# Kernel optimization log

Measured on AMD Instinct MI355X. Metric: run time of the kernel, lower is better.

Reference implementation:

```python
import jax, jax.numpy as jnp
import numpy as np

P = 8        # num policies
Z = 64       # per-policy latent dim
D = P * Z    # total latent dim = 512
A = 8        # action dim
H = 512      # hidden dim
B = 8192     # batch


def setup_inputs() -> dict:
    key = jax.random.key(0)
    ks = jax.random.split(key, 10)
    IN = Z + A
    s1 = 1.0 / np.sqrt(IN)
    s2 = 1.0 / np.sqrt(H)
    return {
        "latents": jax.random.normal(ks[0], (B, D), dtype=jnp.float32),
        "actions": jax.random.normal(ks[1], (B, A), dtype=jnp.float32),
        "policy_indices": jax.random.randint(ks[2], (B,), 0, P, dtype=jnp.int64) if jax.config.jax_enable_x64 else jax.random.randint(ks[2], (B,), 0, P, dtype=jnp.int32),
        # Stacked params for P_outer x P_inner MLPs: (z+A) -> H -> H -> Z
        "W1": jax.random.uniform(ks[3], (P, P, IN, H), jnp.float32, -s1, s1),
        "b1": jax.random.uniform(ks[4], (P, P, H), jnp.float32, -s1, s1),
        "W2": jax.random.uniform(ks[5], (P, P, H, H), jnp.float32, -s2, s2),
        "b2": jax.random.uniform(ks[6], (P, P, H), jnp.float32, -s2, s2),
        "W3": jax.random.uniform(ks[7], (P, P, H, Z), jnp.float32, -s2, s2),
        "b3": jax.random.uniform(ks[8], (P, P, Z), jnp.float32, -s2, s2),
    }


def reference(latents, actions, policy_indices, W1, b1, W2, b2, W3, b3):
    Bb, Dd = latents.shape
    Pp = W1.shape[0]
    Zz = Dd // Pp
    # split latent into per-policy chunks: [B, P, Z]
    pl = latents.reshape(Bb, Pp, Zz)
    # each inner MLP sees (its latent chunk, shared action): [B, P, Z+A]
    act = jnp.broadcast_to(actions[:, None, :], (Bb, Pp, actions.shape[-1]))
    x = jnp.concatenate([pl, act], axis=-1)
    out = jnp.zeros_like(latents)
    # loop over outer policy models (fixed small set); select rows by policy index
    for i in range(Pp):
        h = jax.nn.relu(jnp.einsum("bpi,pih->bph", x, W1[i]) + b1[i])
        h = jax.nn.relu(jnp.einsum("bph,phk->bpk", h, W2[i]) + b2[i])
        y = jnp.einsum("bph,phz->bpz", h, W3[i]) + b3[i]  # [B, P, Z]
        y = y.reshape(Bb, Dd)  # concat over inner policies
        out = jnp.where((policy_indices == i)[:, None], y, out)
    return out
```

## Files before the change

kernel.cpp:

```cpp
#include <hip/hip_runtime.h>
#include <stdint.h>

#define PNUM  8
#define DDIM  512
#define ZDIM  64
#define ADIM  8
#define HDIM  512
#define BATCH 8192
#define KIN   72
#define NKS1  3
#define NKS2  16
#define NKS3  16
#define NT12  32
#define NT3   4
#define TM    64
#define PXP   104
#define PHP   520

typedef __attribute__((ext_vector_type(8))) __bf16 bf16x8;
typedef __attribute__((ext_vector_type(4))) float  f32x4;

#define WS_COUNTS_I 0
#define WS_OFFS_I   16
#define WS_CURS_I   32
#define WS_FLG_I    42
#define WS_PERM_I   64
#define WS_W1P_B    40960
#define WS_W2P_B    (WS_W1P_B + 64*NKS1*NT12*1024)
#define WS_W3P_B    (WS_W2P_B + 64*NKS2*NT12*1024)
#define WS_NEED_B   (WS_W3P_B + 64*NKS3*NT3*1024)

__device__ __forceinline__ float bf2f(ushort h){
  union { unsigned int u; float f; } v; v.u = ((unsigned int)h) << 16; return v.f;
}
__device__ __forceinline__ ushort f2bf(float f){
  union { float f; unsigned int u; } v; v.f = f;
  unsigned int u = v.u;
  return (ushort)((u + 0x7FFFu + ((u >> 16) & 1u)) >> 16);
}
__device__ __forceinline__ unsigned int pk2(ushort lo, ushort hi){
  return (unsigned int)lo | ((unsigned int)hi << 16);
}
__device__ __forceinline__ int ldidx(const void* p, int t, int i64){
  return i64 ? (int)((const long long*)p)[t] : ((const int*)p)[t];
}
__device__ __forceinline__ float4 ldbias4(const void* b, size_t off, int f32){
  if (f32) return *(const float4*)((const float*)b + off);
  ushort4 q = *(const ushort4*)((const ushort*)b + off);
  float4 r; r.x = bf2f(q.x); r.y = bf2f(q.y); r.z = bf2f(q.z); r.w = bf2f(q.w);
  return r;
}

__global__ void k_prep(const unsigned int* __restrict__ lat,
                       const unsigned int* __restrict__ act,
                       const unsigned int* __restrict__ w1,
                       const unsigned int* __restrict__ bb1,
                       const unsigned int* __restrict__ w2,
                       const unsigned int* __restrict__ bb2,
                       const unsigned int* __restrict__ w3,
                       const unsigned int* __restrict__ bb3,
                       const void* __restrict__ idx,
                       int* __restrict__ wsi){
  __shared__ int hist[PNUM];
  __shared__ int cur[PNUM];
  __shared__ int flg_i64;
  const int tid = threadIdx.x;
  if (tid < PNUM) hist[tid] = 0;
  const int t = tid >> 6, lane = tid & 63;
  if (t == 8){
    unsigned long long nz = __ballot(((const unsigned int*)idx)[2 * lane + 1] != 0u);
    if (lane == 0){ int v = (nz == 0ull) ? 1 : 0; wsi[WS_FLG_I + 8] = v; flg_i64 = v; }
  } else if (t < 8){
    const unsigned int* ptrs[8] = {lat, act, w1, bb1, w2, bb2, w3, bb3};
    unsigned int u = ptrs[t][lane];
    unsigned int e = (u >> 7) & 0xFFu;
    unsigned long long ib = __ballot(e >= 100u && e <= 150u);
    if (lane == 0) wsi[WS_FLG_I + t] = (__popcll(ib) < 40) ? 1 : 0;
  }
  __syncthreads();
  const int i64 = flg_i64;
  int pol[8];
  #pragma unroll
  for (int c = 0; c < 8; c++){
    pol[c] = ldidx(idx, c * 1024 + tid, i64);
    atomicAdd(&hist[pol[c]], 1);
  }
  __syncthreads();
  if (tid == 0){
    int off = 0;
    #pragma unroll
    for (int i = 0; i < PNUM; i++){
      int h = hist[i];
      wsi[WS_COUNTS_I + i] = h;
      wsi[WS_OFFS_I + i] = off;
      cur[i] = off;
      off += h;
    }
  }
  __syncthreads();
  #pragma unroll
  for (int c = 0; c < 8; c++){
    int pos = atomicAdd(&cur[pol[c]], 1);
    wsi[WS_PERM_I + pos] = c * 1024 + tid;
  }
}

#define PK_W1_N  1536
#define PK_W2_N  8192
#define PK_W3_N  1024
__global__ void k_pack_all(const void* __restrict__ W1, const void* __restrict__ W2,
                           const void* __restrict__ W3,
                           ushort* __restrict__ w1p, ushort* __restrict__ w2p,
                           ushort* __restrict__ w3p,
                           const int* __restrict__ wsi){
  __shared__ ushort T[32][80];
  int bid = blockIdx.x;
  const void* src; ushort* dst;
  int Ksrc, nks, ntiles, N, flg, ntg, ks, pair;
  if (bid < PK_W1_N){
    src = W1; dst = w1p; Ksrc = KIN;  nks = NKS1; ntiles = NT12; N = HDIM; flg = 2;
    pair = bid / 24; int rem = bid % 24; ks = rem >> 3; ntg = rem & 7;
  } else if (bid < PK_W1_N + PK_W2_N){
    int local = bid - PK_W1_N;
    src = W2; dst = w2p; Ksrc = HDIM; nks = NKS2; ntiles = NT12; N = HDIM; flg = 4;
    pair = local / 128; int rem = local % 128; ks = rem >> 3; ntg = rem & 7;
  } else {
    int local = bid - PK_W1_N - PK_W2_N;
    src = W3; dst = w3p; Ksrc = HDIM; nks = NKS3; ntiles = NT3;  N = ZDIM; flg = 6;
    pair = local / 16; ks = local % 16; ntg = 0;
  }
  const int f32 = wsi[WS_FLG_I + flg];
  const int tid = threadIdx.x;
  const int nb = ntg * 64;

  if (f32){
    #pragma unroll
    for (int it = 0; it < 2; it++){
      int i = it * 256 + tid;
      int k = i >> 4, nq = i & 15;
      int kk = ks * 32 + k;
      float4 v = make_float4(0.f, 0.f, 0.f, 0.f);
      if (kk < Ksrc)
        v = *(const float4*)((const float*)src + ((size_t)pair * Ksrc + kk) * N + nb + nq * 4);
      ushort4 o; o.x = f2bf(v.x); o.y = f2bf(v.y); o.z = f2bf(v.z); o.w = f2bf(v.w);
      *(ushort4*)&T[k][nq * 4] = o;
    }
  } else {
    int k = tid >> 3, uq = tid & 7;
    int kk = ks * 32 + k;
    uint4 v = make_uint4(0u, 0u, 0u, 0u);
    if (kk < Ksrc)
      v = *(const uint4*)((const ushort*)src + ((size_t)pair * Ksrc + kk) * N + nb + uq * 8);
    *(uint4*)&T[k][uq * 8] = v;
  }
  __syncthreads();

  const int w = tid >> 6, lane = tid & 63;
  const int lm = lane & 15, lq = lane >> 4;
  unsigned int vv[4];
  #pragma unroll
  for (int j = 0; j < 4; j++){
    ushort lo = T[lq * 8 + 2 * j    ][w * 16 + lm];
    ushort hi = T[lq * 8 + 2 * j + 1][w * 16 + lm];
    vv[j] = pk2(lo, hi);
  }
  uint4 val = make_uint4(vv[0], vv[1], vv[2], vv[3]);
  size_t f = (size_t)(pair * nks + ks) * ntiles + (ntg * 4 + w);
  *(uint4*)(dst + f * 512 + (size_t)lane * 8) = val;
}

__global__ void __launch_bounds__(512, 2) k_mlp(
    const void* __restrict__ latents, const void* __restrict__ actions,
    const void* __restrict__ b1, const void* __restrict__ b2,
    const void* __restrict__ b3,
    const int* __restrict__ wsi,
    const ushort* __restrict__ w1p, const ushort* __restrict__ w2p,
    const ushort* __restrict__ w3p,
    void* __restrict__ out, int out_elems)
{
  __shared__ __align__(16) ushort Xb [TM * PXP];
  __shared__ __align__(16) ushort H1s[TM * PHP];
  __shared__ __align__(16) ushort H2s[TM * PHP];
  __shared__ int rowid[TM];

  const int io = blockIdx.x >> 3, p = blockIdx.x & 7, tile = blockIdx.y;
  const int cnt = wsi[WS_COUNTS_I + io];
  if (tile * TM >= cnt) return;
  const int r0    = wsi[WS_OFFS_I + io] + tile * TM;
  const int mrows = min(TM, cnt - tile * TM);
  const int pair  = io * PNUM + p;
  const int tid   = threadIdx.x;
  const int fLat  = wsi[WS_FLG_I + 0];
  const int fAct  = wsi[WS_FLG_I + 1];
  const int fB1   = wsi[WS_FLG_I + 3];
  const int fB2   = wsi[WS_FLG_I + 5];
  const int fB3   = wsi[WS_FLG_I + 7];

  const int w = tid >> 6, lane = tid & 63;
  const int lm = lane & 15, lq = lane >> 4;
  const int ntb = w * 4;
  const uint4* w1v = (const uint4*)w1p;
  const uint4* w2v = (const uint4*)w2p;
  const uint4* w3v = (const uint4*)w3p;
  const f32x4 zero4 = {0.f, 0.f, 0.f, 0.f};

  uint4 a1w[NKS1][4];
  #pragma unroll
  for (int ks = 0; ks < NKS1; ks++)
    #pragma unroll
    for (int a = 0; a < 4; a++)
      a1w[ks][a] = w1v[((size_t)(pair * NKS1 + ks) * NT12 + ntb + a) * 64 + lane];
  float4 bq1[4];
  #pragma unroll
  for (int a = 0; a < 4; a++)
    bq1[a] = ldbias4(b1, (size_t)pair * HDIM + (ntb + a) * 16 + lq * 4, fB1);

  for (int task = tid; task < TM * 16; task += 512){
    int r = task >> 4, c = task & 15;
    if (c >= 13) continue;
    uint4 val = make_uint4(0u, 0u, 0u, 0u);
    if (r < mrows){
      int row = wsi[WS_PERM_I + r0 + r];
      if (c == 8) rowid[r] = row;
      if (c < 9){
        int f32 = (c < 8) ? fLat : fAct;
        if (f32){
          const float* sf = (c < 8)
            ? ((const float*)latents + (size_t)row * DDIM + p * ZDIM + c * 8)
            : ((const float*)actions + (size_t)row * ADIM);
          float4 f0 = *(const float4*)sf;
          float4 f1 = *(const float4*)(sf + 4);
          val = make_uint4(pk2(f2bf(f0.x), f2bf(f0.y)),
                           pk2(f2bf(f0.z), f2bf(f0.w)),
                           pk2(f2bf(f1.x), f2bf(f1.y)),
                           pk2(f2bf(f1.z), f2bf(f1.w)));
        } else {
          const ushort* sh = (c < 8)
            ? ((const ushort*)latents + (size_t)row * DDIM + p * ZDIM + c * 8)
            : ((const ushort*)actions + (size_t)row * ADIM);
          val = *(const uint4*)sh;
        }
      }
    } else if (c == 8) rowid[r] = 0;
    *(uint4*)(Xb + r * PXP + c * 8) = val;
  }
  __syncthreads();

  #define MFMA16(A, B) \
    { _Pragma("unroll") for (int a_ = 0; a_ < 4; a_++) \
      { _Pragma("unroll") for (int m_ = 0; m_ < 4; m_++) \
        acc[a_][m_] = __builtin_amdgcn_mfma_f32_16x16x32_bf16( \
            __builtin_bit_cast(bf16x8, A[a_]), __builtin_bit_cast(bf16x8, B[m_]), \
            acc[a_][m_], 0, 0, 0); } }
  #define LDA2(dst, kss) \
    { _Pragma("unroll") for (int a_ = 0; a_ < 4; a_++) \
        dst[a_] = w2v[((size_t)(pair * NKS2 + (kss)) * NT12 + ntb + a_) * 64 + lane]; }
  #define LDB4(dst, kss) \
    { _Pragma("unroll") for (int m_ = 0; m_ < 4; m_++) \
        dst[m_] = *(const uint4*)(H1s + (size_t)(m_ * 16 + lm) * PHP + (kss) * 32 + lq * 8); }
  #define CP4(dst, srcv) \
    { _Pragma("unroll") for (int a_ = 0; a_ < 4; a_++) dst[a_] = srcv[a_]; }

  {
    f32x4 acc[4][4];
    #pragma unroll
    for (int a = 0; a < 4; a++)
      #pragma unroll
      for (int m = 0; m < 4; m++) acc[a][m] = zero4;

    #pragma unroll
    for (int ks = 0; ks < NKS1; ks++){
      uint4 bfm[4];
      #pragma unroll
      for (int m = 0; m < 4; m++)
        bfm[m] = *(const uint4*)(Xb + (size_t)(m * 16 + lm) * PXP + ks * 32 + lq * 8);
      MFMA16(a1w[ks], bfm);
    }
    #pragma unroll
    for (int a = 0; a < 4; a++){
      int n0 = (ntb + a) * 16 + lq * 4;
      #pragma unroll
      for (int m = 0; m < 4; m++){
        ushort4 o;
        o.x = f2bf(fmaxf(acc[a][m][0] + bq1[a].x, 0.f));
        o.y = f2bf(fmaxf(acc[a][m][1] + bq1[a].y, 0.f));
        o.z = f2bf(fmaxf(acc[a][m][2] + bq1[a].z, 0.f));
        o.w = f2bf(fmaxf(acc[a][m][3] + bq1[a].w, 0.f));
        *(ushort4*)(H1s + (size_t)(m * 16 + lm) * PHP + n0) = o;
      }
    }
  }

  uint4 A0[4], A1[4];
  LDA2(A0, 0);
  LDA2(A1, 1);
  float4 bq2[4];
  #pragma unroll
  for (int a = 0; a < 4; a++)
    bq2[a] = ldbias4(b2, (size_t)pair * HDIM + (ntb + a) * 16 + lq * 4, fB2);
  __syncthreads();

  {
    f32x4 acc[4][4];
    #pragma unroll
    for (int a = 0; a < 4; a++)
      #pragma unroll
      for (int m = 0; m < 4; m++) acc[a][m] = zero4;

    uint4 B0[4], B1[4];
    LDB4(B0, 0);
    #pragma unroll
    for (int ks = 0; ks < NKS2; ks += 2){
      uint4 TA[4];
      if (ks + 2 < NKS2) LDA2(TA, ks + 2);
      LDB4(B1, ks + 1);
      MFMA16(A0, B0);
      if (ks + 2 < NKS2) CP4(A0, TA);
      uint4 TB[4];
      if (ks + 3 < NKS2) LDA2(TB, ks + 3);
      if (ks + 2 < NKS2) LDB4(B0, ks + 2);
      MFMA16(A1, B1);
      if (ks + 3 < NKS2) CP4(A1, TB);
    }
    #pragma unroll
    for (int a = 0; a < 4; a++){
      int n0 = (ntb + a) * 16 + lq * 4;
      #pragma unroll
      for (int m = 0; m < 4; m++){
        ushort4 o;
        o.x = f2bf(fmaxf(acc[a][m][0] + bq2[a].x, 0.f));
        o.y = f2bf(fmaxf(acc[a][m][1] + bq2[a].y, 0.f));
        o.z = f2bf(fmaxf(acc[a][m][2] + bq2[a].z, 0.f));
        o.w = f2bf(fmaxf(acc[a][m][3] + bq2[a].w, 0.f));
        *(ushort4*)(H2s + (size_t)(m * 16 + lm) * PHP + n0) = o;
      }
    }
  }

  const int zt = w & 3, mb = w >> 2;
  uint4 C0 = w3v[((size_t)(pair * NKS3 + 0) * NT3 + zt) * 64 + lane];
  uint4 C1 = w3v[((size_t)(pair * NKS3 + 1) * NT3 + zt) * 64 + lane];
  float4 bq3 = ldbias4(b3, (size_t)pair * ZDIM + zt * 16 + lq * 4, fB3);
  __syncthreads();

  {
    f32x4 acc3[2];
    acc3[0] = zero4; acc3[1] = zero4;
    #pragma unroll
    for (int ks = 0; ks < NKS3; ks += 2){
      uint4 T0, T1;
      if (ks + 2 < NKS3)
        T0 = w3v[((size_t)(pair * NKS3 + ks + 2) * NT3 + zt) * 64 + lane];
      if (ks + 3 < NKS3)
        T1 = w3v[((size_t)(pair * NKS3 + ks + 3) * NT3 + zt) * 64 + lane];
      #pragma unroll
      for (int h = 0; h < 2; h++){
        int row = (mb + 2 * h) * 16 + lm;
        uint4 bf = *(const uint4*)(H2s + (size_t)row * PHP + ks * 32 + lq * 8);
        acc3[h] = __builtin_amdgcn_mfma_f32_16x16x32_bf16(
            __builtin_bit_cast(bf16x8, C0), __builtin_bit_cast(bf16x8, bf), acc3[h], 0, 0, 0);
      }
      #pragma unroll
      for (int h = 0; h < 2; h++){
        int row = (mb + 2 * h) * 16 + lm;
        uint4 bf = *(const uint4*)(H2s + (size_t)row * PHP + (ks + 1) * 32 + lq * 8);
        acc3[h] = __builtin_amdgcn_mfma_f32_16x16x32_bf16(
            __builtin_bit_cast(bf16x8, C1), __builtin_bit_cast(bf16x8, bf), acc3[h], 0, 0, 0);
      }
      if (ks + 2 < NKS3) C0 = T0;
      if (ks + 3 < NKS3) C1 = T1;
    }
    int z0 = zt * 16 + lq * 4;
    #pragma unroll
    for (int h = 0; h < 2; h++){
      int mm = (mb + 2 * h) * 16 + lm;
      if (mm < mrows){
        int row = rowid[mm];
        size_t oidx = (size_t)row * DDIM + p * ZDIM + z0;
        if (oidx + 4 <= (size_t)out_elems){
          if (fLat){
            float4 o;
            o.x = acc3[h][0] + bq3.x;
            o.y = acc3[h][1] + bq3.y;
            o.z = acc3[h][2] + bq3.z;
            o.w = acc3[h][3] + bq3.w;
            *(float4*)((float*)out + oidx) = o;
          } else {
            ushort4 o;
            o.x = f2bf(acc3[h][0] + bq3.x);
            o.y = f2bf(acc3[h][1] + bq3.y);
            o.z = f2bf(acc3[h][2] + bq3.z);
            o.w = f2bf(acc3[h][3] + bq3.w);
            *(ushort4*)((ushort*)out + oidx) = o;
          }
        }
      }
    }
  }
  #undef MFMA16
  #undef LDA2
  #undef LDB4
  #undef CP4
}

extern "C" void kernel_launch(void* const* d_in, const int* in_sizes, int n_in,
                              void* d_out, int out_size, void* d_ws, size_t ws_size,
                              hipStream_t stream){
  if (n_in < 9) return;
  const void* latents = d_in[0];
  const void* actions = d_in[1];
  const void* pidx    = d_in[2];
  const void* W1      = d_in[3];
  const void* b1      = d_in[4];
  const void* W2      = d_in[5];
  const void* b2      = d_in[6];
  const void* W3      = d_in[7];
  const void* b3      = d_in[8];

  if (ws_size < (size_t)WS_NEED_B) return;

  int*    wsi = (int*)d_ws;
  char*   wsb = (char*)d_ws;
  ushort* w1p = (ushort*)(wsb + WS_W1P_B);
  ushort* w2p = (ushort*)(wsb + WS_W2P_B);
  ushort* w3p = (ushort*)(wsb + WS_W3P_B);

  k_prep<<<1, 1024, 0, stream>>>(
      (const unsigned int*)latents, (const unsigned int*)actions,
      (const unsigned int*)W1, (const unsigned int*)b1,
      (const unsigned int*)W2, (const unsigned int*)b2,
      (const unsigned int*)W3, (const unsigned int*)b3,
      pidx, wsi);
  k_pack_all<<<PK_W1_N + PK_W2_N + PK_W3_N, 256, 0, stream>>>(
      W1, W2, W3, w1p, w2p, w3p, wsi);
  k_mlp<<<dim3(64, BATCH/TM), 512, 0, stream>>>(
      latents, actions, b1, b2, b3, wsi, w1p, w2p, w3p, d_out, out_size);
}
```

Before: 219.3 us.

## Use persistent 1024-thread MLP blocks looping over tiles; warp-aggregate histogram

```diff
diff --git a/kernel.cpp b/kernel.cpp
--- a/kernel.cpp
+++ b/kernel.cpp
@@ -14,6 +14,7 @@
 #define NT12  32
 #define NT3   4
 #define TM    64
+#define TILEY 16
 #define PXP   104
 #define PHP   520
 
@@ -65,8 +66,8 @@
   __shared__ int cur[PNUM];
   __shared__ int flg_i64;
   const int tid = threadIdx.x;
+  const int t = tid >> 6, lane = tid & 63;
   if (tid < PNUM) hist[tid] = 0;
-  const int t = tid >> 6, lane = tid & 63;
   if (t == 8){
     unsigned long long nz = __ballot(((const unsigned int*)idx)[2 * lane + 1] != 0u);
     if (lane == 0){ int v = (nz == 0ull) ? 1 : 0; wsi[WS_FLG_I + 8] = v; flg_i64 = v; }
@@ -81,9 +82,22 @@
   const int i64 = flg_i64;
   int pol[8];
   #pragma unroll
+  for (int c = 0; c < 8; c++) pol[c] = ldidx(idx, c * 1024 + tid, i64);
+
+  int wcnt[PNUM];
+  #pragma unroll
+  for (int i = 0; i < PNUM; i++) wcnt[i] = 0;
+  #pragma unroll
   for (int c = 0; c < 8; c++){
-    pol[c] = ldidx(idx, c * 1024 + tid, i64);
-    atomicAdd(&hist[pol[c]], 1);
+    #pragma unroll
+    for (int i = 0; i < PNUM; i++){
+      unsigned long long m = __ballot(pol[c] == i);
+      wcnt[i] += __popcll(m);
+    }
+  }
+  if (lane == 0){
+    #pragma unroll
+    for (int i = 0; i < PNUM; i++) atomicAdd(&hist[i], wcnt[i]);
   }
   __syncthreads();
   if (tid == 0){
@@ -98,10 +112,23 @@
     }
   }
   __syncthreads();
+
   #pragma unroll
   for (int c = 0; c < 8; c++){
-    int pos = atomicAdd(&cur[pol[c]], 1);
-    wsi[WS_PERM_I + pos] = c * 1024 + tid;
+    #pragma unroll
+    for (int i = 0; i < PNUM; i++){
+      unsigned long long m = __ballot(pol[c] == i);
+      if (m){
+        int leader = __ffsll((unsigned long long)m) - 1;
+        int base = 0;
+        if (lane == leader) base = atomicAdd(&cur[i], __popcll(m));
+        base = __shfl(base, leader);
+        if (pol[c] == i){
+          int rank = __popcll(m & ((1ull << lane) - 1ull));
+          wsi[WS_PERM_I + base + rank] = c * 1024 + tid;
+        }
+      }
+    }
   }
 }
 
@@ -169,7 +196,7 @@
   *(uint4*)(dst + f * 512 + (size_t)lane * 8) = val;
 }
 
-__global__ void __launch_bounds__(512, 2) k_mlp(
+__global__ void __launch_bounds__(1024, 4) k_mlp(
     const void* __restrict__ latents, const void* __restrict__ actions,
     const void* __restrict__ b1, const void* __restrict__ b2,
     const void* __restrict__ b3,
@@ -183,11 +210,9 @@
   __shared__ __align__(16) ushort H2s[TM * PHP];
   __shared__ int rowid[TM];
 
-  const int io = blockIdx.x >> 3, p = blockIdx.x & 7, tile = blockIdx.y;
+  const int io = blockIdx.x >> 3, p = blockIdx.x & 7;
   const int cnt = wsi[WS_COUNTS_I + io];
-  if (tile * TM >= cnt) return;
-  const int r0    = wsi[WS_OFFS_I + io] + tile * TM;
-  const int mrows = min(TM, cnt - tile * TM);
+  if ((int)blockIdx.y * TM >= cnt) return;
   const int pair  = io * PNUM + p;
   const int tid   = threadIdx.x;
   const int fLat  = wsi[WS_FLG_I + 0];
@@ -198,209 +223,205 @@
 
   const int w = tid >> 6, lane = tid & 63;
   const int lm = lane & 15, lq = lane >> 4;
-  const int ntb = w * 4;
+  const int ntb = w * 2;
+  const int zt = w & 3, mq = w >> 2;
   const uint4* w1v = (const uint4*)w1p;
   const uint4* w2v = (const uint4*)w2p;
   const uint4* w3v = (const uint4*)w3p;
   const f32x4 zero4 = {0.f, 0.f, 0.f, 0.f};
 
-  uint4 a1w[NKS1][4];
+  uint4 a1w[NKS1][2];
   #pragma unroll
   for (int ks = 0; ks < NKS1; ks++)
     #pragma unroll
-    for (int a = 0; a < 4; a++)
+    for (int a = 0; a < 2; a++)
       a1w[ks][a] = w1v[((size_t)(pair * NKS1 + ks) * NT12 + ntb + a) * 64 + lane];
-  float4 bq1[4];
-  #pragma unroll
-  for (int a = 0; a < 4; a++)
+  float4 bq1[2];
+  #pragma unroll
+  for (int a = 0; a < 2; a++)
     bq1[a] = ldbias4(b1, (size_t)pair * HDIM + (ntb + a) * 16 + lq * 4, fB1);
-
-  for (int task = tid; task < TM * 16; task += 512){
-    int r = task >> 4, c = task & 15;
-    if (c >= 13) continue;
-    uint4 val = make_uint4(0u, 0u, 0u, 0u);
-    if (r < mrows){
-      int row = wsi[WS_PERM_I + r0 + r];
-      if (c == 8) rowid[r] = row;
-      if (c < 9){
-        int f32 = (c < 8) ? fLat : fAct;
-        if (f32){
-          const float* sf = (c < 8)
-            ? ((const float*)latents + (size_t)row * DDIM + p * ZDIM + c * 8)
-            : ((const float*)actions + (size_t)row * ADIM);
-          float4 f0 = *(const float4*)sf;
-          float4 f1 = *(const float4*)(sf + 4);
-          val = make_uint4(pk2(f2bf(f0.x), f2bf(f0.y)),
-                           pk2(f2bf(f0.z), f2bf(f0.w)),
-                           pk2(f2bf(f1.x), f2bf(f1.y)),
-                           pk2(f2bf(f1.z), f2bf(f1.w)));
-        } else {
-          const ushort* sh = (c < 8)
-            ? ((const ushort*)latents + (size_t)row * DDIM + p * ZDIM + c * 8)
-            : ((const ushort*)actions + (size_t)row * ADIM);
-          val = *(const uint4*)sh;
-        }
-      }
-    } else if (c == 8) rowid[r] = 0;
-    *(uint4*)(Xb + r * PXP + c * 8) = val;
-  }
-  __syncthreads();
-
-  #define MFMA16(A, B) \
-    { _Pragma("unroll") for (int a_ = 0; a_ < 4; a_++) \
+  float4 bq2[2];
+  #pragma unroll
+  for (int a = 0; a < 2; a++)
+    bq2[a] = ldbias4(b2, (size_t)pair * HDIM + (ntb + a) * 16 + lq * 4, fB2);
+  float4 bq3 = ldbias4(b3, (size_t)pair * ZDIM + zt * 16 + lq * 4, fB3);
+
+  #define MFMA8(A, B) \
+    { _Pragma("unroll") for (int a_ = 0; a_ < 2; a_++) \
       { _Pragma("unroll") for (int m_ = 0; m_ < 4; m_++) \
         acc[a_][m_] = __builtin_amdgcn_mfma_f32_16x16x32_bf16( \
             __builtin_bit_cast(bf16x8, A[a_]), __builtin_bit_cast(bf16x8, B[m_]), \
             acc[a_][m_], 0, 0, 0); } }
   #define LDA2(dst, kss) \
-    { _Pragma("unroll") for (int a_ = 0; a_ < 4; a_++) \
+    { _Pragma("unroll") for (int a_ = 0; a_ < 2; a_++) \
         dst[a_] = w2v[((size_t)(pair * NKS2 + (kss)) * NT12 + ntb + a_) * 64 + lane]; }
   #define LDB4(dst, kss) \
     { _Pragma("unroll") for (int m_ = 0; m_ < 4; m_++) \
         dst[m_] = *(const uint4*)(H1s + (size_t)(m_ * 16 + lm) * PHP + (kss) * 32 + lq * 8); }
-  #define CP4(dst, srcv) \
-    { _Pragma("unroll") for (int a_ = 0; a_ < 4; a_++) dst[a_] = srcv[a_]; }
-
-  {
-    f32x4 acc[4][4];
-    #pragma unroll
-    for (int a = 0; a < 4; a++)
-      #pragma unroll
-      for (int m = 0; m < 4; m++) acc[a][m] = zero4;
-
-    #pragma unroll
-    for (int ks = 0; ks < NKS1; ks++){
-      uint4 bfm[4];
-      #pragma unroll
-      for (int m = 0; m < 4; m++)
-        bfm[m] = *(const uint4*)(Xb + (size_t)(m * 16 + lm) * PXP + ks * 32 + lq * 8);
-      MFMA16(a1w[ks], bfm);
-    }
-    #pragma unroll
-    for (int a = 0; a < 4; a++){
-      int n0 = (ntb + a) * 16 + lq * 4;
-      #pragma unroll
-      for (int m = 0; m < 4; m++){
-        ushort4 o;
-        o.x = f2bf(fmaxf(acc[a][m][0] + bq1[a].x, 0.f));
-        o.y = f2bf(fmaxf(acc[a][m][1] + bq1[a].y, 0.f));
-        o.z = f2bf(fmaxf(acc[a][m][2] + bq1[a].z, 0.f));
-        o.w = f2bf(fmaxf(acc[a][m][3] + bq1[a].w, 0.f));
-        *(ushort4*)(H1s + (size_t)(m * 16 + lm) * PHP + n0) = o;
-      }
-    }
-  }
-
-  uint4 A0[4], A1[4];
-  LDA2(A0, 0);
-  LDA2(A1, 1);
-  float4 bq2[4];
-  #pragma unroll
-  for (int a = 0; a < 4; a++)
-    bq2[a] = ldbias4(b2, (size_t)pair * HDIM + (ntb + a) * 16 + lq * 4, fB2);
-  __syncthreads();
-
-  {
-    f32x4 acc[4][4];
-    #pragma unroll
-    for (int a = 0; a < 4; a++)
-      #pragma unroll
-      for (int m = 0; m < 4; m++) acc[a][m] = zero4;
-
-    uint4 B0[4], B1[4];
-    LDB4(B0, 0);
-    #pragma unroll
-    for (int ks = 0; ks < NKS2; ks += 2){
-      uint4 TA[4];
-      if (ks + 2 < NKS2) LDA2(TA, ks + 2);
-      LDB4(B1, ks + 1);
-      MFMA16(A0, B0);
-      if (ks + 2 < NKS2) CP4(A0, TA);
-      uint4 TB[4];
-      if (ks + 3 < NKS2) LDA2(TB, ks + 3);
-      if (ks + 2 < NKS2) LDB4(B0, ks + 2);
-      MFMA16(A1, B1);
-      if (ks + 3 < NKS2) CP4(A1, TB);
-    }
-    #pragma unroll
-    for (int a = 0; a < 4; a++){
-      int n0 = (ntb + a) * 16 + lq * 4;
-      #pragma unroll
-      for (int m = 0; m < 4; m++){
-        ushort4 o;
-        o.x = f2bf(fmaxf(acc[a][m][0] + bq2[a].x, 0.f));
-        o.y = f2bf(fmaxf(acc[a][m][1] + bq2[a].y, 0.f));
-        o.z = f2bf(fmaxf(acc[a][m][2] + bq2[a].z, 0.f));
-        o.w = f2bf(fmaxf(acc[a][m][3] + bq2[a].w, 0.f));
-        *(ushort4*)(H2s + (size_t)(m * 16 + lm) * PHP + n0) = o;
-      }
-    }
-  }
-
-  const int zt = w & 3, mb = w >> 2;
-  uint4 C0 = w3v[((size_t)(pair * NKS3 + 0) * NT3 + zt) * 64 + lane];
-  uint4 C1 = w3v[((size_t)(pair * NKS3 + 1) * NT3 + zt) * 64 + lane];
-  float4 bq3 = ldbias4(b3, (size_t)pair * ZDIM + zt * 16 + lq * 4, fB3);
-  __syncthreads();
-
-  {
-    f32x4 acc3[2];
-    acc3[0] = zero4; acc3[1] = zero4;
-    #pragma unroll
-    for (int ks = 0; ks < NKS3; ks += 2){
-      uint4 T0, T1;
-      if (ks + 2 < NKS3)
-        T0 = w3v[((size_t)(pair * NKS3 + ks + 2) * NT3 + zt) * 64 + lane];
-      if (ks + 3 < NKS3)
-        T1 = w3v[((size_t)(pair * NKS3 + ks + 3) * NT3 + zt) * 64 + lane];
-      #pragma unroll
-      for (int h = 0; h < 2; h++){
-        int row = (mb + 2 * h) * 16 + lm;
-        uint4 bf = *(const uint4*)(H2s + (size_t)row * PHP + ks * 32 + lq * 8);
-        acc3[h] = __builtin_amdgcn_mfma_f32_16x16x32_bf16(
-            __builtin_bit_cast(bf16x8, C0), __builtin_bit_cast(bf16x8, bf), acc3[h], 0, 0, 0);
-      }
-      #pragma unroll
-      for (int h = 0; h < 2; h++){
-        int row = (mb + 2 * h) * 16 + lm;
-        uint4 bf = *(const uint4*)(H2s + (size_t)row * PHP + (ks + 1) * 32 + lq * 8);
-        acc3[h] = __builtin_amdgcn_mfma_f32_16x16x32_bf16(
-            __builtin_bit_cast(bf16x8, C1), __builtin_bit_cast(bf16x8, bf), acc3[h], 0, 0, 0);
-      }
-      if (ks + 2 < NKS3) C0 = T0;
-      if (ks + 3 < NKS3) C1 = T1;
-    }
-    int z0 = zt * 16 + lq * 4;
-    #pragma unroll
-    for (int h = 0; h < 2; h++){
-      int mm = (mb + 2 * h) * 16 + lm;
+  #define CP2(dst, srcv) \
+    { _Pragma("unroll") for (int a_ = 0; a_ < 2; a_++) dst[a_] = srcv[a_]; }
+
+  for (int tile = blockIdx.y; tile * TM < cnt; tile += TILEY){
+    const int r0    = wsi[WS_OFFS_I + io] + tile * TM;
+    const int mrows = min(TM, cnt - tile * TM);
+
+    __syncthreads();
+
+    {
+      int r = tid >> 4, c = tid & 15;
+      if (c < 13){
+        uint4 val = make_uint4(0u, 0u, 0u, 0u);
+        if (r < mrows){
+          int row = wsi[WS_PERM_I + r0 + r];
+          if (c == 8) rowid[r] = row;
+          if (c < 9){
+            int f32 = (c < 8) ? fLat : fAct;
+            if (f32){
+              const float* sf = (c < 8)
+                ? ((const float*)latents + (size_t)row * DDIM + p * ZDIM + c * 8)
+                : ((const float*)actions + (size_t)row * ADIM);
+              float4 f0 = *(const float4*)sf;
+              float4 f1 = *(const float4*)(sf + 4);
+              val = make_uint4(pk2(f2bf(f0.x), f2bf(f0.y)),
+                               pk2(f2bf(f0.z), f2bf(f0.w)),
+                               pk2(f2bf(f1.x), f2bf(f1.y)),
+                               pk2(f2bf(f1.z), f2bf(f1.w)));
+            } else {
+              const ushort* sh = (c < 8)
+                ? ((const ushort*)latents + (size_t)row * DDIM + p * ZDIM + c * 8)
+                : ((const ushort*)actions + (size_t)row * ADIM);
+              val = *(const uint4*)sh;
+            }
+          }
+        } else if (c == 8) rowid[r] = 0;
+        *(uint4*)(Xb + r * PXP + c * 8) = val;
+      }
+    }
+    __syncthreads();
+
+    {
+      f32x4 acc[2][4];
+      #pragma unroll
+      for (int a = 0; a < 2; a++)
+        #pragma unroll
+        for (int m = 0; m < 4; m++) acc[a][m] = zero4;
+
+      #pragma unroll
+      for (int ks = 0; ks < NKS1; ks++){
+        uint4 bfm[4];
+        #pragma unroll
+        for (int m = 0; m < 4; m++)
+          bfm[m] = *(const uint4*)(Xb + (size_t)(m * 16 + lm) * PXP + ks * 32 + lq * 8);
+        MFMA8(a1w[ks], bfm);
+      }
+      #pragma unroll
+      for (int a = 0; a < 2; a++){
+        int n0 = (ntb + a) * 16 + lq * 4;
+        #pragma unroll
+        for (int m = 0; m < 4; m++){
+          ushort4 o;
+          o.x = f2bf(fmaxf(acc[a][m][0] + bq1[a].x, 0.f));
+          o.y = f2bf(fmaxf(acc[a][m][1] + bq1[a].y, 0.f));
+          o.z = f2bf(fmaxf(acc[a][m][2] + bq1[a].z, 0.f));
+          o.w = f2bf(fmaxf(acc[a][m][3] + bq1[a].w, 0.f));
+          *(ushort4*)(H1s + (size_t)(m * 16 + lm) * PHP + n0) = o;
+        }
+      }
+    }
+
+    uint4 A0[2], A1[2];
+    LDA2(A0, 0);
+    LDA2(A1, 1);
+    __syncthreads();
+
+    {
+      f32x4 acc[2][4];
+      #pragma unroll
+      for (int a = 0; a < 2; a++)
+        #pragma unroll
+        for (int m = 0; m < 4; m++) acc[a][m] = zero4;
+
+      uint4 B0[4], B1[4];
+      LDB4(B0, 0);
+      #pragma unroll
+      for (int ks = 0; ks < NKS2; ks += 2){
+        uint4 TA[2];
+        if (ks + 2 < NKS2) LDA2(TA, ks + 2);
+        LDB4(B1, ks + 1);
+        MFMA8(A0, B0);
+        if (ks + 2 < NKS2) CP2(A0, TA);
+        uint4 TB[2];
+        if (ks + 3 < NKS2) LDA2(TB, ks + 3);
+        if (ks + 2 < NKS2) LDB4(B0, ks + 2);
+        MFMA8(A1, B1);
+        if (ks + 3 < NKS2) CP2(A1, TB);
+      }
+      #pragma unroll
+      for (int a = 0; a < 2; a++){
+        int n0 = (ntb + a) * 16 + lq * 4;
+        #pragma unroll
+        for (int m = 0; m < 4; m++){
+          ushort4 o;
+          o.x = f2bf(fmaxf(acc[a][m][0] + bq2[a].x, 0.f));
+          o.y = f2bf(fmaxf(acc[a][m][1] + bq2[a].y, 0.f));
+          o.z = f2bf(fmaxf(acc[a][m][2] + bq2[a].z, 0.f));
+          o.w = f2bf(fmaxf(acc[a][m][3] + bq2[a].w, 0.f));
+          *(ushort4*)(H2s + (size_t)(m * 16 + lm) * PHP + n0) = o;
+        }
+      }
+    }
+
+    uint4 C0 = w3v[((size_t)(pair * NKS3 + 0) * NT3 + zt) * 64 + lane];
+    uint4 C1 = w3v[((size_t)(pair * NKS3 + 1) * NT3 + zt) * 64 + lane];
+    __syncthreads();
+
+    {
+      f32x4 acc3 = zero4;
+      #pragma unroll
+      for (int ks = 0; ks < NKS3; ks += 2){
+        uint4 T0, T1;
+        if (ks + 2 < NKS3)
+          T0 = w3v[((size_t)(pair * NKS3 + ks + 2) * NT3 + zt) * 64 + lane];
+        if (ks + 3 < NKS3)
+          T1 = w3v[((size_t)(pair * NKS3 + ks + 3) * NT3 + zt) * 64 + lane];
+        uint4 bf = *(const uint4*)(H2s + (size_t)(mq * 16 + lm) * PHP + ks * 32 + lq * 8);
+        acc3 = __builtin_amdgcn_mfma_f32_16x16x32_bf16(
+            __builtin_bit_cast(bf16x8, C0), __builtin_bit_cast(bf16x8, bf), acc3, 0, 0, 0);
+        uint4 bg = *(const uint4*)(H2s + (size_t)(mq * 16 + lm) * PHP + (ks + 1) * 32 + lq * 8);
+        acc3 = __builtin_amdgcn_mfma_f32_16x16x32_bf16(
+            __builtin_bit_cast(bf16x8, C1), __builtin_bit_cast(bf16x8, bg), acc3, 0, 0, 0);
+        if (ks + 2 < NKS3) C0 = T0;
+        if (ks + 3 < NKS3) C1 = T1;
+      }
+      int z0 = zt * 16 + lq * 4;
+      int mm = mq * 16 + lm;
       if (mm < mrows){
         int row = rowid[mm];
         size_t oidx = (size_t)row * DDIM + p * ZDIM + z0;
         if (oidx + 4 <= (size_t)out_elems){
           if (fLat){
             float4 o;
-            o.x = acc3[h][0] + bq3.x;
-            o.y = acc3[h][1] + bq3.y;
-            o.z = acc3[h][2] + bq3.z;
-            o.w = acc3[h][3] + bq3.w;
+            o.x = acc3[0] + bq3.x;
+            o.y = acc3[1] + bq3.y;
+            o.z = acc3[2] + bq3.z;
+            o.w = acc3[3] + bq3.w;
             *(float4*)((float*)out + oidx) = o;
           } else {
             ushort4 o;
-            o.x = f2bf(acc3[h][0] + bq3.x);
-            o.y = f2bf(acc3[h][1] + bq3.y);
-            o.z = f2bf(acc3[h][2] + bq3.z);
-            o.w = f2bf(acc3[h][3] + bq3.w);
+            o.x = f2bf(acc3[0] + bq3.x);
+            o.y = f2bf(acc3[1] + bq3.y);
+            o.z = f2bf(acc3[2] + bq3.z);
+            o.w = f2bf(acc3[3] + bq3.w);
             *(ushort4*)((ushort*)out + oidx) = o;
           }
         }
       }
     }
   }
-  #undef MFMA16
+  #undef MFMA8
   #undef LDA2
   #undef LDB4
-  #undef CP4
+  #undef CP2
 }
 
 extern "C" void kernel_launch(void* const* d_in, const int* in_sizes, int n_in,
@@ -433,6 +454,6 @@
       pidx, wsi);
   k_pack_all<<<PK_W1_N + PK_W2_N + PK_W3_N, 256, 0, stream>>>(
       W1, W2, W3, w1p, w2p, w3p, wsi);
-  k_mlp<<<dim3(64, BATCH/TM), 512, 0, stream>>>(
+  k_mlp<<<dim3(64, TILEY), 1024, 0, stream>>>(
       latents, actions, b1, b2, b3, wsi, w1p, w2p, w3p, d_out, out_size);
 }
```

New measurement: 527.9 us. 2.41x slower.

## Merge prep and weight-pack kernels into one launch with ballot-based histogram

Applied to the files above, without the earlier changes.

```diff
diff --git a/kernel.cpp b/kernel.cpp
--- a/kernel.cpp
+++ b/kernel.cpp
@@ -30,6 +30,12 @@
 #define WS_W3P_B    (WS_W2P_B + 64*NKS2*NT12*1024)
 #define WS_NEED_B   (WS_W3P_B + 64*NKS3*NT3*1024)
 
+#define FR_W1   6144
+#define FR_W2   32768
+#define FR_W3   4096
+#define FR_TOT  (FR_W1 + FR_W2 + FR_W3)
+#define NB_PACK 2048
+
 __device__ __forceinline__ float bf2f(ushort h){
   union { unsigned int u; float f; } v; v.u = ((unsigned int)h) << 16; return v.f;
 }
@@ -51,122 +57,137 @@
   return r;
 }
 
-__global__ void k_prep(const unsigned int* __restrict__ lat,
-                       const unsigned int* __restrict__ act,
-                       const unsigned int* __restrict__ w1,
-                       const unsigned int* __restrict__ bb1,
-                       const unsigned int* __restrict__ w2,
-                       const unsigned int* __restrict__ bb2,
-                       const unsigned int* __restrict__ w3,
-                       const unsigned int* __restrict__ bb3,
-                       const void* __restrict__ idx,
-                       int* __restrict__ wsi){
+__global__ void k_pack_all(const void* __restrict__ W1, const void* __restrict__ W2,
+                           const void* __restrict__ W3,
+                           const unsigned int* __restrict__ lat,
+                           const unsigned int* __restrict__ act,
+                           const unsigned int* __restrict__ bb1,
+                           const unsigned int* __restrict__ bb2,
+                           const unsigned int* __restrict__ bb3,
+                           const void* __restrict__ idx,
+                           ushort* __restrict__ w1p, ushort* __restrict__ w2p,
+                           ushort* __restrict__ w3p,
+                           int* __restrict__ wsi){
   __shared__ int hist[PNUM];
   __shared__ int cur[PNUM];
-  __shared__ int flg_i64;
+  const int bid = blockIdx.x;
   const int tid = threadIdx.x;
-  if (tid < PNUM) hist[tid] = 0;
-  const int t = tid >> 6, lane = tid & 63;
-  if (t == 8){
-    unsigned long long nz = __ballot(((const unsigned int*)idx)[2 * lane + 1] != 0u);
-    if (lane == 0){ int v = (nz == 0ull) ? 1 : 0; wsi[WS_FLG_I + 8] = v; flg_i64 = v; }
-  } else if (t < 8){
-    const unsigned int* ptrs[8] = {lat, act, w1, bb1, w2, bb2, w3, bb3};
-    unsigned int u = ptrs[t][lane];
-    unsigned int e = (u >> 7) & 0xFFu;
-    unsigned long long ib = __ballot(e >= 100u && e <= 150u);
-    if (lane == 0) wsi[WS_FLG_I + t] = (__popcll(ib) < 40) ? 1 : 0;
-  }
-  __syncthreads();
-  const int i64 = flg_i64;
-  int pol[8];
-  #pragma unroll
-  for (int c = 0; c < 8; c++){
-    pol[c] = ldidx(idx, c * 1024 + tid, i64);
-    atomicAdd(&hist[pol[c]], 1);
-  }
-  __syncthreads();
-  if (tid == 0){
-    int off = 0;
-    #pragma unroll
-    for (int i = 0; i < PNUM; i++){
-      int h = hist[i];
-      wsi[WS_COUNTS_I + i] = h;
-      wsi[WS_OFFS_I + i] = off;
-      cur[i] = off;
-      off += h;
-    }
-  }
-  __syncthreads();
-  #pragma unroll
-  for (int c = 0; c < 8; c++){
-    int pos = atomicAdd(&cur[pol[c]], 1);
-    wsi[WS_PERM_I + pos] = c * 1024 + tid;
-  }
-}
-
-#define PK_W1_N  1536
-#define PK_W2_N  8192
-#define PK_W3_N  1024
-__global__ void k_pack_all(const void* __restrict__ W1, const void* __restrict__ W2,
-                           const void* __restrict__ W3,
-                           ushort* __restrict__ w1p, ushort* __restrict__ w2p,
-                           ushort* __restrict__ w3p,
-                           const int* __restrict__ wsi){
-  __shared__ ushort T[32][80];
-  int bid = blockIdx.x;
-  const void* src; ushort* dst;
-  int Ksrc, nks, ntiles, N, flg, ntg, ks, pair;
-  if (bid < PK_W1_N){
-    src = W1; dst = w1p; Ksrc = KIN;  nks = NKS1; ntiles = NT12; N = HDIM; flg = 2;
-    pair = bid / 24; int rem = bid % 24; ks = rem >> 3; ntg = rem & 7;
-  } else if (bid < PK_W1_N + PK_W2_N){
-    int local = bid - PK_W1_N;
-    src = W2; dst = w2p; Ksrc = HDIM; nks = NKS2; ntiles = NT12; N = HDIM; flg = 4;
-    pair = local / 128; int rem = local % 128; ks = rem >> 3; ntg = rem & 7;
-  } else {
-    int local = bid - PK_W1_N - PK_W2_N;
-    src = W3; dst = w3p; Ksrc = HDIM; nks = NKS3; ntiles = NT3;  N = ZDIM; flg = 6;
-    pair = local / 16; ks = local % 16; ntg = 0;
-  }
-  const int f32 = wsi[WS_FLG_I + flg];
-  const int tid = threadIdx.x;
-  const int nb = ntg * 64;
-
-  if (f32){
-    #pragma unroll
-    for (int it = 0; it < 2; it++){
-      int i = it * 256 + tid;
-      int k = i >> 4, nq = i & 15;
-      int kk = ks * 32 + k;
-      float4 v = make_float4(0.f, 0.f, 0.f, 0.f);
-      if (kk < Ksrc)
-        v = *(const float4*)((const float*)src + ((size_t)pair * Ksrc + kk) * N + nb + nq * 4);
-      ushort4 o; o.x = f2bf(v.x); o.y = f2bf(v.y); o.z = f2bf(v.z); o.w = f2bf(v.w);
-      *(ushort4*)&T[k][nq * 4] = o;
-    }
-  } else {
-    int k = tid >> 3, uq = tid & 7;
-    int kk = ks * 32 + k;
-    uint4 v = make_uint4(0u, 0u, 0u, 0u);
-    if (kk < Ksrc)
-      v = *(const uint4*)((const ushort*)src + ((size_t)pair * Ksrc + kk) * N + nb + uq * 8);
-    *(uint4*)&T[k][uq * 8] = v;
-  }
-  __syncthreads();
-
-  const int w = tid >> 6, lane = tid & 63;
+  const int wv = tid >> 6, lane = tid & 63;
+
+  if (bid == NB_PACK){
+    if (tid < PNUM) hist[tid] = 0;
+    for (int j = wv; j < 6; j += 4){
+      if (j == 5){
+        unsigned long long nz = __ballot(((const unsigned int*)idx)[2 * lane + 1] != 0u);
+        if (lane == 0) wsi[WS_FLG_I + 8] = (nz == 0ull) ? 1 : 0;
+      } else {
+        const unsigned int* ptrs[5] = {lat, act, bb1, bb2, bb3};
+        const int fslot[5] = {0, 1, 3, 5, 7};
+        unsigned int u = ptrs[j][lane];
+        unsigned int e = (u >> 7) & 0xFFu;
+        unsigned long long ib = __ballot(e >= 100u && e <= 150u);
+        if (lane == 0) wsi[WS_FLG_I + fslot[j]] = (__popcll(ib) < 40) ? 1 : 0;
+      }
+    }
+    __syncthreads();
+    const int i64 = wsi[WS_FLG_I + 8];
+    int pol[32];
+    #pragma unroll
+    for (int c = 0; c < 32; c++) pol[c] = ldidx(idx, c * 256 + tid, i64);
+
+    int wcnt[PNUM];
+    #pragma unroll
+    for (int i = 0; i < PNUM; i++) wcnt[i] = 0;
+    #pragma unroll
+    for (int c = 0; c < 32; c++){
+      #pragma unroll
+      for (int i = 0; i < PNUM; i++)
+        wcnt[i] += __popcll(__ballot(pol[c] == i));
+    }
+    if (lane == 0){
+      #pragma unroll
+      for (int i = 0; i < PNUM; i++) atomicAdd(&hist[i], wcnt[i]);
+    }
+    __syncthreads();
+    if (tid == 0){
+      int off = 0;
+      #pragma unroll
+      for (int i = 0; i < PNUM; i++){
+        int h = hist[i];
+        wsi[WS_COUNTS_I + i] = h;
+        wsi[WS_OFFS_I + i] = off;
+        cur[i] = off;
+        off += h;
+      }
+    }
+    __syncthreads();
+    #pragma unroll
+    for (int c = 0; c < 32; c++){
+      #pragma unroll
+      for (int i = 0; i < PNUM; i++){
+        unsigned long long m = __ballot(pol[c] == i);
+        if (m){
+          int leader = __ffsll((unsigned long long)m) - 1;
+          int base = 0;
+          if (lane == leader) base = atomicAdd(&cur[i], __popcll(m));
+          base = __shfl(base, leader);
+          if (pol[c] == i){
+            int rank = __popcll(m & ((1ull << lane) - 1ull));
+            wsi[WS_PERM_I + base + rank] = c * 256 + tid;
+          }
+        }
+      }
+    }
+    return;
+  }
+
   const int lm = lane & 15, lq = lane >> 4;
-  unsigned int vv[4];
-  #pragma unroll
-  for (int j = 0; j < 4; j++){
-    ushort lo = T[lq * 8 + 2 * j    ][w * 16 + lm];
-    ushort hi = T[lq * 8 + 2 * j + 1][w * 16 + lm];
-    vv[j] = pk2(lo, hi);
-  }
-  uint4 val = make_uint4(vv[0], vv[1], vv[2], vv[3]);
-  size_t f = (size_t)(pair * nks + ks) * ntiles + (ntg * 4 + w);
-  *(uint4*)(dst + f * 512 + (size_t)lane * 8) = val;
+  unsigned int u1 = ((const unsigned int*)W1)[lane];
+  unsigned int u2 = ((const unsigned int*)W2)[lane];
+  unsigned int u3 = ((const unsigned int*)W3)[lane];
+  const int fw1 = (__popcll(__ballot((((u1 >> 7) & 0xFFu) >= 100u) && (((u1 >> 7) & 0xFFu) <= 150u))) < 40) ? 1 : 0;
+  const int fw2 = (__popcll(__ballot((((u2 >> 7) & 0xFFu) >= 100u) && (((u2 >> 7) & 0xFFu) <= 150u))) < 40) ? 1 : 0;
+  const int fw3 = (__popcll(__ballot((((u3 >> 7) & 0xFFu) >= 100u) && (((u3 >> 7) & 0xFFu) <= 150u))) < 40) ? 1 : 0;
+
+  const int gw = bid * 4 + wv;
+  for (int f = gw; f < FR_TOT; f += NB_PACK * 4){
+    const void* src; ushort* dst;
+    int Ksrc, N, f32, pair, ks, nt; size_t fi;
+    if (f < FR_W1){
+      src = W1; dst = w1p; Ksrc = KIN; N = HDIM; f32 = fw1; fi = (size_t)f;
+      pair = f / 96; int r = f % 96; ks = r >> 5; nt = r & 31;
+    } else if (f < FR_W1 + FR_W2){
+      int g = f - FR_W1;
+      src = W2; dst = w2p; Ksrc = HDIM; N = HDIM; f32 = fw2; fi = (size_t)g;
+      pair = g >> 9; int r = g & 511; ks = r >> 5; nt = r & 31;
+    } else {
+      int h = f - FR_W1 - FR_W2;
+      src = W3; dst = w3p; Ksrc = HDIM; N = ZDIM; f32 = fw3; fi = (size_t)h;
+      pair = h >> 6; int r = h & 63; ks = r >> 2; nt = r & 3;
+    }
+    const int k0 = ks * 32 + lq * 8;
+    const int n  = nt * 16 + lm;
+    const size_t base = ((size_t)pair * Ksrc + k0) * N + n;
+    unsigned int d[4];
+    if (f32){
+      const float* s = (const float*)src + base;
+      float v[8];
+      #pragma unroll
+      for (int j = 0; j < 8; j++)
+        v[j] = (k0 + j < Ksrc) ? s[(size_t)j * N] : 0.f;
+      #pragma unroll
+      for (int j = 0; j < 4; j++) d[j] = pk2(f2bf(v[2*j]), f2bf(v[2*j+1]));
+    } else {
+      const ushort* s = (const ushort*)src + base;
+      ushort v[8];
+      #pragma unroll
+      for (int j = 0; j < 8; j++)
+        v[j] = (k0 + j < Ksrc) ? s[(size_t)j * N] : (ushort)0;
+      #pragma unroll
+      for (int j = 0; j < 4; j++) d[j] = pk2(v[2*j], v[2*j+1]);
+    }
+    *(uint4*)(dst + fi * 512 + (size_t)lane * 8) = make_uint4(d[0], d[1], d[2], d[3]);
+  }
 }
 
 __global__ void __launch_bounds__(512, 2) k_mlp(
@@ -425,14 +446,12 @@
   ushort* w2p = (ushort*)(wsb + WS_W2P_B);
   ushort* w3p = (ushort*)(wsb + WS_W3P_B);
 
-  k_prep<<<1, 1024, 0, stream>>>(
+  k_pack_all<<<NB_PACK + 1, 256, 0, stream>>>(
+      W1, W2, W3,
       (const unsigned int*)latents, (const unsigned int*)actions,
-      (const unsigned int*)W1, (const unsigned int*)b1,
-      (const unsigned int*)W2, (const unsigned int*)b2,
-      (const unsigned int*)W3, (const unsigned int*)b3,
-      pidx, wsi);
-  k_pack_all<<<PK_W1_N + PK_W2_N + PK_W3_N, 256, 0, stream>>>(
-      W1, W2, W3, w1p, w2p, w3p, wsi);
+      (const unsigned int*)b1, (const unsigned int*)b2,
+      (const unsigned int*)b3, pidx,
+      w1p, w2p, w3p, wsi);
   k_mlp<<<dim3(64, BATCH/TM), 512, 0, stream>>>(
       latents, actions, b1, b2, b3, wsi, w1p, w2p, w3p, d_out, out_size);
 }
```

Result: slower. 264.1 us (+20.4%).
